# Optimization experiments

Hardware: AMD Instinct MI355X
Metric: run time of the kernel (lower is better)

Reference implementation:

```python
import jax, jax.numpy as jnp
import numpy as np

HID = 512
HEADS = 8
HEAD_DIM = HID // HEADS
BS, SEQ = 4, 2048


def setup_inputs() -> dict:
    key = jax.random.key(0)
    ks = jax.random.split(key, 12)
    s = 0.02
    return {
        "query": jax.random.normal(ks[0], (BS, SEQ, HID), jnp.float32),
        "key": jax.random.normal(ks[1], (BS, SEQ, HID), jnp.float32),
        "value": jax.random.normal(ks[2], (BS, SEQ, HID), jnp.float32),
        "query_mask": jnp.ones((BS, SEQ), dtype=bool),
        "key_mask": jnp.ones((BS, SEQ), dtype=bool),
        "Wq": jax.random.normal(ks[3], (HID, HID), jnp.float32) * s,
        "bq": jnp.zeros((HID,), jnp.float32),
        "Wk": jax.random.normal(ks[4], (HID, HID), jnp.float32) * s,
        "bk": jnp.zeros((HID,), jnp.float32),
        "Wv": jax.random.normal(ks[5], (HID, HID), jnp.float32) * s,
        "bv": jnp.zeros((HID,), jnp.float32),
        "Wo": jax.random.normal(ks[6], (HID, HID), jnp.float32) * s,
        "bo": jnp.zeros((HID,), jnp.float32),
    }


def _mha(query, key, value, query_mask, key_mask, Wq, bq, Wk, bk, Wv, bv, Wo, bo):
    bs, q_len, _ = query.shape
    k_len = key.shape[1]
    scale = jnp.sqrt(jnp.asarray(HEAD_DIM, query.dtype))

    def proj(x, W, b):  # nn.Linear: x @ W^T + b, then split heads -> [b,h,s,d]
        y = jnp.einsum('bse,fe->bsf', x, W) + b
        return y.reshape(bs, -1, HEADS, HEAD_DIM).transpose(0, 2, 1, 3)

    q = proj(query, Wq, bq)
    k = proj(key, Wk, bk)
    v = proj(value, Wv, bv)

    energy = jnp.einsum('bhqd,bhkd->bhqk', q, k) / scale  # [b,h,q,k]
    neg = -jnp.finfo(energy.dtype).max

    pad_mask = query_mask[:, None, :, None] & key_mask[:, None, None, :]
    energy = jnp.where(pad_mask, energy, neg)

    # causal: mask positions where q_idx < k_idx
    causal = jnp.arange(q_len)[:, None] < jnp.arange(k_len)[None, :]
    energy = jnp.where(causal[None, None], neg, energy)

    attn = jax.nn.softmax(energy, axis=-1)  # dropout p=0.0 -> identity
    x = jnp.einsum('bhqk,bhkd->bhqd', attn, v)
    x = x.transpose(0, 2, 1, 3).reshape(bs, q_len, HID)
    return jnp.einsum('bse,fe->bsf', x, Wo) + bo


def reference(query, key, value, query_mask, key_mask, Wq, bq, Wk, bk, Wv, bv, Wo, bo):
    return _mha(query, key, value, query_mask, key_mask, Wq, bq, Wk, bk, Wv, bv, Wo, bo)
```

## Files before the change

### kernel.cpp

```cpp
#include <hip/hip_runtime.h>
#include <hip/hip_bf16.h>

#define DEVI __device__ __forceinline__

typedef __attribute__((ext_vector_type(4)))  float f32x4;
typedef __attribute__((ext_vector_type(16))) float f32x16;
typedef __attribute__((ext_vector_type(8)))  short bf16x8;

constexpr int BS    = 4;
constexpr int SEQ   = 2048;
constexpr int HID   = 512;
constexpr int HEADS = 8;
constexpr int HD    = 64;
constexpr int M     = BS * SEQ;

constexpr float QSCALE = 0.125f * 1.4426950408889634f;

DEVI ushort f2bf(float f) {
    union { float f; unsigned u; } a; a.f = f;
    unsigned r = a.u + 0x7fffu + ((a.u >> 16) & 1u);
    return (ushort)(r >> 16);
}

DEVI f32x4 mfma16(bf16x8 a, bf16x8 b, f32x4 c) {
    return __builtin_amdgcn_mfma_f32_16x16x32_bf16(a, b, c, 0, 0, 0);
}
DEVI f32x16 mfma32(bf16x8 a, bf16x8 b, f32x16 c) {
    return __builtin_amdgcn_mfma_f32_32x32x16_bf16(a, b, c, 0, 0, 0);
}

DEVI void gl_lds16(const ushort* g, ushort* l) {
    __builtin_amdgcn_global_load_lds(
        (const __attribute__((address_space(1))) void*)g,
        (__attribute__((address_space(3))) void*)l,
        16, 0, 0);
}

DEVI unsigned cvtpk(float lo, float hi) {
    unsigned r;
    asm("v_cvt_pk_bf16_f32 %0, %1, %2" : "=v"(r) : "v"(lo), "v"(hi));
    return r;
}

__global__ void cast_w(const float* __restrict__ wq, const float* __restrict__ wk,
                       const float* __restrict__ wv, const float* __restrict__ wo,
                       ushort* __restrict__ oq, ushort* __restrict__ ok,
                       ushort* __restrict__ ov, ushort* __restrict__ oo)
{
    const int NW4 = HID * HID / 4;
    int i = blockIdx.x * blockDim.x + threadIdx.x;
    const int a = i >> 16, j = i & (NW4 - 1);
    const float* src = (a == 0) ? wq : (a == 1) ? wk : (a == 2) ? wv : wo;
    ushort* dst = (a == 0) ? oq : (a == 1) ? ok : (a == 2) ? ov : oo;
    float4 f = ((const float4*)src)[j];
    ushort4 u;
    u.x = f2bf(f.x); u.y = f2bf(f.y); u.z = f2bf(f.z); u.w = f2bf(f.w);
    ((ushort4*)dst)[j] = u;
}

template<bool AF32>
DEVI void gemm_core(const void* __restrict__ Ain, const ushort* __restrict__ W,
                    const float* __restrict__ bias, void* __restrict__ out,
                    float scale, int mode, ushort* lA, ushort* lB)
{
    constexpr int BK = 32, NK = HID / BK;
    const int tid  = threadIdx.x;
    const int lane = tid & 63, w = tid >> 6;
    const int wm = w >> 2, wn = w & 3;
    const int l15 = lane & 15, lg = lane >> 4;
    const int m0 = blockIdx.x * 128, n0 = blockIdx.y * 128;
    const int srow = tid >> 2, sc8 = (tid & 3) * 8;

    f32x4 acc[4][2];
    #pragma unroll
    for (int i = 0; i < 4; i++)
        #pragma unroll
        for (int n = 0; n < 2; n++) acc[i][n] = f32x4{0.f, 0.f, 0.f, 0.f};

    if constexpr (AF32) {
        const float* A = (const float*)Ain;
        const float4* ap = (const float4*)(A + (size_t)(m0 + srow) * HID + sc8);
        const float4 a0 = ap[0], a1 = ap[1];
        union { unsigned u[4]; bf16x8 v; } p;
        p.u[0] = cvtpk(a0.x, a0.y); p.u[1] = cvtpk(a0.z, a0.w);
        p.u[2] = cvtpk(a1.x, a1.y); p.u[3] = cvtpk(a1.z, a1.w);
        *(bf16x8*)(lA + srow * 32 + sc8) = p.v;
    } else {
        gl_lds16((const ushort*)Ain + (size_t)(m0 + srow) * HID + sc8, lA + w * 512);
    }
    gl_lds16(W + (size_t)(n0 + srow) * HID + sc8, lB + w * 512);
    __syncthreads();

    int cur = 0;
    for (int k = 0; k < NK; ++k) {
        ushort* lAc = lA + cur * 4096;
        ushort* lBc = lB + cur * 4096;
        ushort* lAn = lA + (cur ^ 1) * 4096;
        ushort* lBn = lB + (cur ^ 1) * 4096;
        const int k1 = (k + 1) * BK;
        const bool more = (k + 1 < NK);

        float4 a0n, a1n;
        if (more) {
            if constexpr (AF32) {
                const float* A = (const float*)Ain;
                const float4* ap = (const float4*)(A + (size_t)(m0 + srow) * HID + k1 + sc8);
                a0n = ap[0]; a1n = ap[1];
            } else {
                gl_lds16((const ushort*)Ain + (size_t)(m0 + srow) * HID + k1 + sc8,
                         lAn + w * 512);
            }
            gl_lds16(W + (size_t)(n0 + srow) * HID + k1 + sc8, lBn + w * 512);
        }

        bf16x8 af[4], bfr[2];
        #pragma unroll
        for (int i = 0; i < 4; i++)
            af[i] = *(const bf16x8*)(lAc + (wm * 64 + i * 16 + l15) * 32 + lg * 8);
        #pragma unroll
        for (int n = 0; n < 2; n++)
            bfr[n] = *(const bf16x8*)(lBc + (wn * 32 + n * 16 + l15) * 32 + lg * 8);
        #pragma unroll
        for (int i = 0; i < 4; i++)
            #pragma unroll
            for (int n = 0; n < 2; n++)
                acc[i][n] = mfma16(af[i], bfr[n], acc[i][n]);

        if (more) {
            if constexpr (AF32) {
                union { unsigned u[4]; bf16x8 v; } p;
                p.u[0] = cvtpk(a0n.x, a0n.y); p.u[1] = cvtpk(a0n.z, a0n.w);
                p.u[2] = cvtpk(a1n.x, a1n.y); p.u[3] = cvtpk(a1n.z, a1n.w);
                *(bf16x8*)(lAn + srow * 32 + sc8) = p.v;
            }
        }
        __syncthreads();
        cur ^= 1;
    }

    #pragma unroll
    for (int i = 0; i < 4; i++) {
        #pragma unroll
        for (int n = 0; n < 2; n++) {
            const int col = n0 + wn * 32 + n * 16 + l15;
            const float bb = bias[col];
            const int rbase = m0 + wm * 64 + i * 16 + lg * 4;
            #pragma unroll
            for (int jj = 0; jj < 4; jj++) {
                float v = (acc[i][n][jj] + bb) * scale;
                const int r = rbase + jj;
                if (mode == 3) {
                    ((float*)out)[(size_t)r * HID + col] = v;
                } else {
                    const int b = r >> 11, s = r & (SEQ - 1);
                    const int h = col >> 6, d = col & 63;
                    const int bh = b * HEADS + h;
                    const int t = s >> 5;
                    const ushort u = f2bf(v);
                    if (mode == 0) {
                        const int l31r = s & 31;
                        const int ds = d >> 4, hif = (d >> 3) & 1, jf = d & 7;
                        ((ushort*)out)[(((size_t)bh * 64 + t) * 4 + ds) * 512 +
                                       (hif * 32 + l31r) * 8 + jf] = u;
                    } else {
                        const int c = s & 31;
                        const int kvh = (c >> 4) & 1, hif = (c >> 2) & 1;
                        const int jf = (c & 3) + ((c >> 3) & 1) * 4;
                        const int dt = d >> 5, drow = d & 31;
                        ((ushort*)out)[(((size_t)bh * 64 + t) * 4 + dt * 2 + kvh) * 512 +
                                       (hif * 32 + drow) * 8 + jf] = u;
                    }
                }
            }
        }
    }
}

__global__ __launch_bounds__(512, 4)
void gemm_qkv(const float* __restrict__ Xq, const float* __restrict__ Xk,
              const float* __restrict__ Xv,
              const ushort* __restrict__ Wq, const ushort* __restrict__ Wk,
              const ushort* __restrict__ Wv,
              const float* __restrict__ bq, const float* __restrict__ bk,
              const float* __restrict__ bv,
              ushort* __restrict__ Qf, ushort* __restrict__ Kf,
              ushort* __restrict__ Vf)
{
    __shared__ ushort lA[2 * 128 * 32];
    __shared__ ushort lB[2 * 128 * 32];
    const int z = blockIdx.z;
    const float* A = z == 0 ? Xq : z == 1 ? Xk : Xv;
    const ushort* W = z == 0 ? Wq : z == 1 ? Wk : Wv;
    const float* bias = z == 0 ? bq : z == 1 ? bk : bv;
    void* out = z == 0 ? (void*)Qf : z == 1 ? (void*)Kf : (void*)Vf;
    gemm_core<true>(A, W, bias, out, z == 0 ? QSCALE : 1.0f, z == 2 ? 2 : 0, lA, lB);
}

__global__ __launch_bounds__(512, 4)
void gemm_o(const ushort* __restrict__ ctx, const ushort* __restrict__ Wo,
            const float* __restrict__ bo, float* __restrict__ out)
{
    __shared__ ushort lA[2 * 128 * 32];
    __shared__ ushort lB[2 * 128 * 32];
    gemm_core<false>(ctx, Wo, bo, out, 1.0f, 3, lA, lB);
}

__global__ __launch_bounds__(256)
void attn5(const ushort* __restrict__ Qf, const ushort* __restrict__ Kf,
           const ushort* __restrict__ Vf, ushort* __restrict__ ctx)
{
    __shared__ float part[4][2][16][64];
    __shared__ float pml[4][2][32];

    const int tid  = threadIdx.x;
    const int lane = tid & 63, w = tid >> 6;
    const int l31 = lane & 31, hi = lane >> 5;

    const int bid = blockIdx.x;
    const int bh  = bid & 31;
    const int qt  = 63 - (bid >> 5);
    const int qb  = qt * 32;

    const ushort* Qb = Qf + ((size_t)bh * 64 + qt) * 2048;
    const ushort* Kb = Kf + (size_t)bh * 64 * 2048;
    const ushort* Vb = Vf + (size_t)bh * 64 * 2048;

    bf16x8 qf[4];
    #pragma unroll
    for (int ds = 0; ds < 4; ds++)
        qf[ds] = *(const bf16x8*)(Qb + ds * 512 + lane * 8);

    f32x16 acc0 = {}, acc1 = {};
    float mrun = -3e38f, lrun = 0.f;

    bf16x8 kf[4] = {}, va[4] = {};
    if (w <= qt) {
        const ushort* kp = Kb + (size_t)w * 2048 + lane * 8;
        const ushort* vp = Vb + (size_t)w * 2048 + lane * 8;
        #pragma unroll
        for (int ds = 0; ds < 4; ds++) {
            kf[ds] = *(const bf16x8*)(kp + ds * 512);
            va[ds] = *(const bf16x8*)(vp + ds * 512);
        }
    }

    for (int t = w; t <= qt; t += 4) {
        f32x16 s = {};
        #pragma unroll
        for (int ds = 0; ds < 4; ds++)
            s = mfma32(kf[ds], qf[ds], s);

        bf16x8 kfn[4], van[4];
        {
            const int tn = (t + 4 <= qt) ? t + 4 : t;
            const ushort* kp = Kb + (size_t)tn * 2048 + lane * 8;
            const ushort* vp = Vb + (size_t)tn * 2048 + lane * 8;
            #pragma unroll
            for (int ds = 0; ds < 4; ds++) {
                kfn[ds] = *(const bf16x8*)(kp + ds * 512);
                van[ds] = *(const bf16x8*)(vp + ds * 512);
            }
        }

        if (t == qt) {
            #pragma unroll
            for (int r = 0; r < 16; r++) {
                const int kvrow = (r & 3) + 8 * (r >> 2) + 4 * hi;
                s[r] = (kvrow > l31) ? -3e38f : s[r];
            }
        }

        float m8[8];
        #pragma unroll
        for (int r = 0; r < 8; r++) m8[r] = fmaxf(s[r], s[r + 8]);
        float m4a = fmaxf(m8[0], m8[1]), m4b = fmaxf(m8[2], m8[3]);
        float m4c = fmaxf(m8[4], m8[5]), m4d = fmaxf(m8[6], m8[7]);
        float pmax = fmaxf(fmaxf(m4a, m4b), fmaxf(m4c, m4d));
        pmax = fmaxf(pmax, __shfl_xor(pmax, 32));

        if (!__all(pmax <= mrun + 8.f)) {
            const float mnew = fmaxf(mrun, pmax);
            const float corr = __builtin_amdgcn_exp2f(mrun - mnew);
            lrun *= corr;
            #pragma unroll
            for (int r = 0; r < 16; r++) { acc0[r] *= corr; acc1[r] *= corr; }
            mrun = mnew;
        }

        float e[16];
        #pragma unroll
        for (int r = 0; r < 16; r++)
            e[r] = __builtin_amdgcn_exp2f(s[r] - mrun);
        float es0 = (e[0] + e[1]) + (e[2] + e[3]);
        float es1 = (e[4] + e[5]) + (e[6] + e[7]);
        float es2 = (e[8] + e[9]) + (e[10] + e[11]);
        float es3 = (e[12] + e[13]) + (e[14] + e[15]);
        float esum = (es0 + es1) + (es2 + es3);
        lrun += esum + __shfl_xor(esum, 32);

        union { unsigned u[4]; bf16x8 v; } pb0, pb1;
        pb0.u[0] = cvtpk(e[0],  e[1]);  pb0.u[1] = cvtpk(e[2],  e[3]);
        pb0.u[2] = cvtpk(e[4],  e[5]);  pb0.u[3] = cvtpk(e[6],  e[7]);
        pb1.u[0] = cvtpk(e[8],  e[9]);  pb1.u[1] = cvtpk(e[10], e[11]);
        pb1.u[2] = cvtpk(e[12], e[13]); pb1.u[3] = cvtpk(e[14], e[15]);

        acc0 = mfma32(va[0], pb0.v, acc0);
        acc0 = mfma32(va[1], pb1.v, acc0);
        acc1 = mfma32(va[2], pb0.v, acc1);
        acc1 = mfma32(va[3], pb1.v, acc1);

        #pragma unroll
        for (int ds = 0; ds < 4; ds++) { kf[ds] = kfn[ds]; va[ds] = van[ds]; }
    }

    #pragma unroll
    for (int r = 0; r < 16; r++) {
        part[w][0][r][lane] = acc0[r];
        part[w][1][r][lane] = acc1[r];
    }
    if (hi == 0) { pml[w][0][l31] = mrun; pml[w][1][l31] = lrun; }
    __syncthreads();

    const float mm0 = pml[0][0][l31], ll0 = pml[0][1][l31];
    const float mm1 = pml[1][0][l31], ll1 = pml[1][1][l31];
    const float mm2 = pml[2][0][l31], ll2 = pml[2][1][l31];
    const float mm3 = pml[3][0][l31], ll3 = pml[3][1][l31];
    const float mstar = fmaxf(fmaxf(mm0, mm1), fmaxf(mm2, mm3));
    const float f0 = __builtin_amdgcn_exp2f(mm0 - mstar);
    const float f1 = __builtin_amdgcn_exp2f(mm1 - mstar);
    const float f2 = __builtin_amdgcn_exp2f(mm2 - mstar);
    const float f3 = __builtin_amdgcn_exp2f(mm3 - mstar);
    const float lstar = ll0 * f0 + ll1 * f1 + ll2 * f2 + ll3 * f3;
    const float inv = 1.f / lstar;

    const int b = bh >> 3, h = bh & 7;
    ushort* op = ctx + ((size_t)(b * SEQ + qb + l31)) * HID + h * HD;
    #pragma unroll
    for (int a = 0; a < 2; a++) {
        float v[4];
        #pragma unroll
        for (int j = 0; j < 4; j++) {
            const int r = 4 * w + j;
            v[j] = (part[0][a][r][lane] * f0 + part[1][a][r][lane] * f1 +
                    part[2][a][r][lane] * f2 + part[3][a][r][lane] * f3) * inv;
        }
        ushort4 o;
        o.x = f2bf(v[0]); o.y = f2bf(v[1]); o.z = f2bf(v[2]); o.w = f2bf(v[3]);
        *(ushort4*)(op + a * 32 + 8 * w + 4 * hi) = o;
    }
}

extern "C" void kernel_launch(void* const* d_in, const int* in_sizes, int n_in,
                              void* d_out, int out_size, void* d_ws, size_t ws_size,
                              hipStream_t stream) {
    const float* q  = (const float*)d_in[0];
    const float* k  = (const float*)d_in[1];
    const float* v  = (const float*)d_in[2];
    const float* Wq = (const float*)d_in[5];
    const float* bq = (const float*)d_in[6];
    const float* Wk = (const float*)d_in[7];
    const float* bk = (const float*)d_in[8];
    const float* Wv = (const float*)d_in[9];
    const float* bv = (const float*)d_in[10];
    const float* Wo = (const float*)d_in[11];
    const float* bo = (const float*)d_in[12];

    char* ws = (char*)d_ws;
    constexpr size_t XSZ = (size_t)M * HID * 2;
    constexpr size_t WSZ = (size_t)HID * HID * 2;
    ushort* Wqb = (ushort*)(ws);
    ushort* Wkb = (ushort*)(ws + WSZ);
    ushort* Wvb = (ushort*)(ws + 2 * WSZ);
    ushort* Wob = (ushort*)(ws + 3 * WSZ);
    ushort* Qf  = (ushort*)(ws + 4 * WSZ);
    ushort* Kf  = (ushort*)(ws + 4 * WSZ + XSZ);
    ushort* Vf  = (ushort*)(ws + 4 * WSZ + 2 * XSZ);
    ushort* ctx = (ushort*)(ws + 4 * WSZ + 3 * XSZ);

    cast_w<<<1024, 256, 0, stream>>>(Wq, Wk, Wv, Wo, Wqb, Wkb, Wvb, Wob);

    dim3 gqkv(M / 128, HID / 128, 3);
    gemm_qkv<<<gqkv, 512, 0, stream>>>(q, k, v, Wqb, Wkb, Wvb,
                                       bq, bk, bv, Qf, Kf, Vf);

    attn5<<<BS * HEADS * (SEQ / 32), 256, 0, stream>>>(Qf, Kf, Vf, ctx);

    dim3 go(M / 128, HID / 128);
    gemm_o<<<go, 512, 0, stream>>>(ctx, Wob, bo, (float*)d_out);
}
```

Before: 91.62 us.

## Process two query tiles per attention block and restructure GEMM LDS pipeline

The attention kernel now handles a 64-row query strip (two 32-row tiles) per block, so each K/V tile loaded from global memory serves two query tiles. This halves the block count and cuts redundant K/V reads, at the cost of more registers and serialized epilogue passes. The GEMM core switches to a fragment-major LDS layout that matches the MFMA operand order, prefetches fp32 A two steps ahead, and replaces __syncthreads with explicit waitcnt plus s_barrier so global loads can stay in flight across iterations.

```diff
diff --git a/kernel.cpp b/kernel.cpp
--- a/kernel.cpp
+++ b/kernel.cpp
@@ -69,7 +69,14 @@
     const int wm = w >> 2, wn = w & 3;
     const int l15 = lane & 15, lg = lane >> 4;
     const int m0 = blockIdx.x * 128, n0 = blockIdx.y * 128;
-    const int srow = tid >> 2, sc8 = (tid & 3) * 8;
+    const int fr = lane & 15;
+    const int fc = (lane >> 4) * 8;
+
+    const ushort* Wrow = W + (size_t)(n0 + 16 * w + fr) * HID + fc;
+    const float*  Af   = (const float*)Ain;
+    const ushort* Ab   = (const ushort*)Ain;
+    const float*  Arow = Af + (size_t)(m0 + 16 * w + fr) * HID + fc;
+    const ushort* Abrow = Ab + (size_t)(m0 + 16 * w + fr) * HID + fc;
 
     f32x4 acc[4][2];
     #pragma unroll
@@ -77,19 +84,23 @@
         #pragma unroll
         for (int n = 0; n < 2; n++) acc[i][n] = f32x4{0.f, 0.f, 0.f, 0.f};
 
+    gl_lds16(Wrow, lB + w * 512);
+    float4 aR0, aR1;
     if constexpr (AF32) {
-        const float* A = (const float*)Ain;
-        const float4* ap = (const float4*)(A + (size_t)(m0 + srow) * HID + sc8);
-        const float4 a0 = ap[0], a1 = ap[1];
+        const float4* ap = (const float4*)Arow;
+        float4 a0 = ap[0], a1 = ap[1];
         union { unsigned u[4]; bf16x8 v; } p;
         p.u[0] = cvtpk(a0.x, a0.y); p.u[1] = cvtpk(a0.z, a0.w);
         p.u[2] = cvtpk(a1.x, a1.y); p.u[3] = cvtpk(a1.z, a1.w);
-        *(bf16x8*)(lA + srow * 32 + sc8) = p.v;
+        *(bf16x8*)(lA + tid * 8) = p.v;
+        const float4* ap1 = (const float4*)(Arow + BK);
+        aR0 = ap1[0]; aR1 = ap1[1];
+        asm volatile("s_waitcnt lgkmcnt(0)" ::: "memory");
     } else {
-        gl_lds16((const ushort*)Ain + (size_t)(m0 + srow) * HID + sc8, lA + w * 512);
-    }
-    gl_lds16(W + (size_t)(n0 + srow) * HID + sc8, lB + w * 512);
-    __syncthreads();
+        gl_lds16(Abrow, lA + w * 512);
+        asm volatile("s_waitcnt vmcnt(0) lgkmcnt(0)" ::: "memory");
+    }
+    __builtin_amdgcn_s_barrier();
 
     int cur = 0;
     for (int k = 0; k < NK; ++k) {
@@ -97,44 +108,44 @@
         ushort* lBc = lB + cur * 4096;
         ushort* lAn = lA + (cur ^ 1) * 4096;
         ushort* lBn = lB + (cur ^ 1) * 4096;
-        const int k1 = (k + 1) * BK;
-        const bool more = (k + 1 < NK);
-
-        float4 a0n, a1n;
-        if (more) {
-            if constexpr (AF32) {
-                const float* A = (const float*)Ain;
-                const float4* ap = (const float4*)(A + (size_t)(m0 + srow) * HID + k1 + sc8);
-                a0n = ap[0]; a1n = ap[1];
-            } else {
-                gl_lds16((const ushort*)Ain + (size_t)(m0 + srow) * HID + k1 + sc8,
-                         lAn + w * 512);
-            }
-            gl_lds16(W + (size_t)(n0 + srow) * HID + k1 + sc8, lBn + w * 512);
+        const bool moreB = (k + 1 < NK);
+        const bool moreA = AF32 && (k + 2 < NK);
+
+        if (moreB) gl_lds16(Wrow + (k + 1) * BK, lBn + w * 512);
+
+        if constexpr (AF32) {
+            if (moreB) {
+                union { unsigned u[4]; bf16x8 v; } p;
+                p.u[0] = cvtpk(aR0.x, aR0.y); p.u[1] = cvtpk(aR0.z, aR0.w);
+                p.u[2] = cvtpk(aR1.x, aR1.y); p.u[3] = cvtpk(aR1.z, aR1.w);
+                *(bf16x8*)(lAn + tid * 8) = p.v;
+            }
+            if (moreA) {
+                const float4* ap = (const float4*)(Arow + (k + 2) * BK);
+                aR0 = ap[0]; aR1 = ap[1];
+            }
+        } else {
+            if (moreB) gl_lds16(Abrow + (k + 1) * BK, lAn + w * 512);
         }
 
         bf16x8 af[4], bfr[2];
         #pragma unroll
         for (int i = 0; i < 4; i++)
-            af[i] = *(const bf16x8*)(lAc + (wm * 64 + i * 16 + l15) * 32 + lg * 8);
+            af[i] = *(const bf16x8*)(lAc + (wm * 4 + i) * 512 + lane * 8);
         #pragma unroll
         for (int n = 0; n < 2; n++)
-            bfr[n] = *(const bf16x8*)(lBc + (wn * 32 + n * 16 + l15) * 32 + lg * 8);
+            bfr[n] = *(const bf16x8*)(lBc + (wn * 2 + n) * 512 + lane * 8);
         #pragma unroll
         for (int i = 0; i < 4; i++)
             #pragma unroll
             for (int n = 0; n < 2; n++)
                 acc[i][n] = mfma16(af[i], bfr[n], acc[i][n]);
 
-        if (more) {
-            if constexpr (AF32) {
-                union { unsigned u[4]; bf16x8 v; } p;
-                p.u[0] = cvtpk(a0n.x, a0n.y); p.u[1] = cvtpk(a0n.z, a0n.w);
-                p.u[2] = cvtpk(a1n.x, a1n.y); p.u[3] = cvtpk(a1n.z, a1n.w);
-                *(bf16x8*)(lAn + srow * 32 + sc8) = p.v;
-            }
-        }
-        __syncthreads();
+        if (moreB) {
+            if (moreA) asm volatile("s_waitcnt vmcnt(2) lgkmcnt(0)" ::: "memory");
+            else       asm volatile("s_waitcnt vmcnt(0) lgkmcnt(0)" ::: "memory");
+            __builtin_amdgcn_s_barrier();
+        }
         cur ^= 1;
     }
 
@@ -186,8 +197,8 @@
               ushort* __restrict__ Qf, ushort* __restrict__ Kf,
               ushort* __restrict__ Vf)
 {
-    __shared__ ushort lA[2 * 128 * 32];
-    __shared__ ushort lB[2 * 128 * 32];
+    __shared__ ushort lA[2 * 8 * 512];
+    __shared__ ushort lB[2 * 8 * 512];
     const int z = blockIdx.z;
     const float* A = z == 0 ? Xq : z == 1 ? Xk : Xv;
     const ushort* W = z == 0 ? Wq : z == 1 ? Wk : Wv;
@@ -200,13 +211,13 @@
 void gemm_o(const ushort* __restrict__ ctx, const ushort* __restrict__ Wo,
             const float* __restrict__ bo, float* __restrict__ out)
 {
-    __shared__ ushort lA[2 * 128 * 32];
-    __shared__ ushort lB[2 * 128 * 32];
+    __shared__ ushort lA[2 * 8 * 512];
+    __shared__ ushort lB[2 * 8 * 512];
     gemm_core<false>(ctx, Wo, bo, out, 1.0f, 3, lA, lB);
 }
 
 __global__ __launch_bounds__(256)
-void attn5(const ushort* __restrict__ Qf, const ushort* __restrict__ Kf,
+void attn6(const ushort* __restrict__ Qf, const ushort* __restrict__ Kf,
            const ushort* __restrict__ Vf, ushort* __restrict__ ctx)
 {
     __shared__ float part[4][2][16][64];
@@ -218,135 +229,181 @@
 
     const int bid = blockIdx.x;
     const int bh  = bid & 31;
-    const int qt  = 63 - (bid >> 5);
-    const int qb  = qt * 32;
-
-    const ushort* Qb = Qf + ((size_t)bh * 64 + qt) * 2048;
+    const int strip = 31 - (bid >> 5);
+    const int qtA = strip * 2, qtB = qtA + 1;
+    const int qbase = strip * 64;
+
     const ushort* Kb = Kf + (size_t)bh * 64 * 2048;
     const ushort* Vb = Vf + (size_t)bh * 64 * 2048;
-
-    bf16x8 qf[4];
+    const ushort* QbA = Qf + ((size_t)bh * 64 + qtA) * 2048;
+    const ushort* QbB = QbA + 2048;
+
+    bf16x8 qfA[4], qfB[4];
     #pragma unroll
-    for (int ds = 0; ds < 4; ds++)
-        qf[ds] = *(const bf16x8*)(Qb + ds * 512 + lane * 8);
-
-    f32x16 acc0 = {}, acc1 = {};
-    float mrun = -3e38f, lrun = 0.f;
-
-    bf16x8 kf[4] = {}, va[4] = {};
-    if (w <= qt) {
+    for (int ds = 0; ds < 4; ds++) {
+        qfA[ds] = *(const bf16x8*)(QbA + ds * 512 + lane * 8);
+        qfB[ds] = *(const bf16x8*)(QbB + ds * 512 + lane * 8);
+    }
+
+    f32x16 a0A = {}, a1A = {}, a0B = {}, a1B = {};
+    float mA = -3e38f, lA_ = 0.f, mB = -3e38f, lB_ = 0.f;
+
+    bf16x8 kf[4] = {};
+    if (w <= qtB) {
         const ushort* kp = Kb + (size_t)w * 2048 + lane * 8;
-        const ushort* vp = Vb + (size_t)w * 2048 + lane * 8;
-        #pragma unroll
-        for (int ds = 0; ds < 4; ds++) {
-            kf[ds] = *(const bf16x8*)(kp + ds * 512);
-            va[ds] = *(const bf16x8*)(vp + ds * 512);
-        }
-    }
-
-    for (int t = w; t <= qt; t += 4) {
-        f32x16 s = {};
-        #pragma unroll
-        for (int ds = 0; ds < 4; ds++)
-            s = mfma32(kf[ds], qf[ds], s);
-
-        bf16x8 kfn[4], van[4];
+        #pragma unroll
+        for (int ds = 0; ds < 4; ds++) kf[ds] = *(const bf16x8*)(kp + ds * 512);
+    }
+
+    for (int t = w; t <= qtB; t += 4) {
+        const bool doA = (t <= qtA);
+
+        f32x16 sB = {};
+        #pragma unroll
+        for (int ds = 0; ds < 4; ds++) sB = mfma32(kf[ds], qfB[ds], sB);
+
+        bf16x8 va[4], kfn[4];
         {
-            const int tn = (t + 4 <= qt) ? t + 4 : t;
+            const ushort* vp = Vb + (size_t)t * 2048 + lane * 8;
+            const int tn = (t + 4 <= qtB) ? t + 4 : t;
             const ushort* kp = Kb + (size_t)tn * 2048 + lane * 8;
-            const ushort* vp = Vb + (size_t)tn * 2048 + lane * 8;
             #pragma unroll
             for (int ds = 0; ds < 4; ds++) {
+                va[ds]  = *(const bf16x8*)(vp + ds * 512);
                 kfn[ds] = *(const bf16x8*)(kp + ds * 512);
-                van[ds] = *(const bf16x8*)(vp + ds * 512);
-            }
-        }
-
-        if (t == qt) {
+            }
+        }
+
+        if (t == qtB) {
             #pragma unroll
             for (int r = 0; r < 16; r++) {
                 const int kvrow = (r & 3) + 8 * (r >> 2) + 4 * hi;
-                s[r] = (kvrow > l31) ? -3e38f : s[r];
-            }
-        }
-
-        float m8[8];
-        #pragma unroll
-        for (int r = 0; r < 8; r++) m8[r] = fmaxf(s[r], s[r + 8]);
-        float m4a = fmaxf(m8[0], m8[1]), m4b = fmaxf(m8[2], m8[3]);
-        float m4c = fmaxf(m8[4], m8[5]), m4d = fmaxf(m8[6], m8[7]);
-        float pmax = fmaxf(fmaxf(m4a, m4b), fmaxf(m4c, m4d));
-        pmax = fmaxf(pmax, __shfl_xor(pmax, 32));
-
-        if (!__all(pmax <= mrun + 8.f)) {
-            const float mnew = fmaxf(mrun, pmax);
-            const float corr = __builtin_amdgcn_exp2f(mrun - mnew);
-            lrun *= corr;
-            #pragma unroll
-            for (int r = 0; r < 16; r++) { acc0[r] *= corr; acc1[r] *= corr; }
-            mrun = mnew;
-        }
-
-        float e[16];
-        #pragma unroll
-        for (int r = 0; r < 16; r++)
-            e[r] = __builtin_amdgcn_exp2f(s[r] - mrun);
-        float es0 = (e[0] + e[1]) + (e[2] + e[3]);
-        float es1 = (e[4] + e[5]) + (e[6] + e[7]);
-        float es2 = (e[8] + e[9]) + (e[10] + e[11]);
-        float es3 = (e[12] + e[13]) + (e[14] + e[15]);
-        float esum = (es0 + es1) + (es2 + es3);
-        lrun += esum + __shfl_xor(esum, 32);
-
-        union { unsigned u[4]; bf16x8 v; } pb0, pb1;
-        pb0.u[0] = cvtpk(e[0],  e[1]);  pb0.u[1] = cvtpk(e[2],  e[3]);
-        pb0.u[2] = cvtpk(e[4],  e[5]);  pb0.u[3] = cvtpk(e[6],  e[7]);
-        pb1.u[0] = cvtpk(e[8],  e[9]);  pb1.u[1] = cvtpk(e[10], e[11]);
-        pb1.u[2] = cvtpk(e[12], e[13]); pb1.u[3] = cvtpk(e[14], e[15]);
-
-        acc0 = mfma32(va[0], pb0.v, acc0);
-        acc0 = mfma32(va[1], pb1.v, acc0);
-        acc1 = mfma32(va[2], pb0.v, acc1);
-        acc1 = mfma32(va[3], pb1.v, acc1);
-
-        #pragma unroll
-        for (int ds = 0; ds < 4; ds++) { kf[ds] = kfn[ds]; va[ds] = van[ds]; }
-    }
-
+                sB[r] = (kvrow > l31) ? -3e38f : sB[r];
+            }
+        }
+
+        union { unsigned u[4]; bf16x8 v; } pb0B, pb1B;
+        {
+            float m8[8];
+            #pragma unroll
+            for (int r = 0; r < 8; r++) m8[r] = fmaxf(sB[r], sB[r + 8]);
+            float pmax = fmaxf(fmaxf(fmaxf(m8[0], m8[1]), fmaxf(m8[2], m8[3])),
+                               fmaxf(fmaxf(m8[4], m8[5]), fmaxf(m8[6], m8[7])));
+            pmax = fmaxf(pmax, __shfl_xor(pmax, 32));
+            if (!__all(pmax <= mB + 8.f)) {
+                const float mnew = fmaxf(mB, pmax);
+                const float corr = __builtin_amdgcn_exp2f(mB - mnew);
+                lB_ *= corr;
+                #pragma unroll
+                for (int r = 0; r < 16; r++) { a0B[r] *= corr; a1B[r] *= corr; }
+                mB = mnew;
+            }
+            float e[16];
+            #pragma unroll
+            for (int r = 0; r < 16; r++) e[r] = __builtin_amdgcn_exp2f(sB[r] - mB);
+            float es = ((e[0]+e[1])+(e[2]+e[3])) + ((e[4]+e[5])+(e[6]+e[7]))
+                     + ((e[8]+e[9])+(e[10]+e[11])) + ((e[12]+e[13])+(e[14]+e[15]));
+            lB_ += es + __shfl_xor(es, 32);
+            pb0B.u[0] = cvtpk(e[0],  e[1]);  pb0B.u[1] = cvtpk(e[2],  e[3]);
+            pb0B.u[2] = cvtpk(e[4],  e[5]);  pb0B.u[3] = cvtpk(e[6],  e[7]);
+            pb1B.u[0] = cvtpk(e[8],  e[9]);  pb1B.u[1] = cvtpk(e[10], e[11]);
+            pb1B.u[2] = cvtpk(e[12], e[13]); pb1B.u[3] = cvtpk(e[14], e[15]);
+        }
+
+        union { unsigned u[4]; bf16x8 v; } pb0A, pb1A;
+        if (doA) {
+            f32x16 sA = {};
+            #pragma unroll
+            for (int ds = 0; ds < 4; ds++) sA = mfma32(kf[ds], qfA[ds], sA);
+            if (t == qtA) {
+                #pragma unroll
+                for (int r = 0; r < 16; r++) {
+                    const int kvrow = (r & 3) + 8 * (r >> 2) + 4 * hi;
+                    sA[r] = (kvrow > l31) ? -3e38f : sA[r];
+                }
+            }
+            float m8[8];
+            #pragma unroll
+            for (int r = 0; r < 8; r++) m8[r] = fmaxf(sA[r], sA[r + 8]);
+            float pmax = fmaxf(fmaxf(fmaxf(m8[0], m8[1]), fmaxf(m8[2], m8[3])),
+                               fmaxf(fmaxf(m8[4], m8[5]), fmaxf(m8[6], m8[7])));
+            pmax = fmaxf(pmax, __shfl_xor(pmax, 32));
+            if (!__all(pmax <= mA + 8.f)) {
+                const float mnew = fmaxf(mA, pmax);
+                const float corr = __builtin_amdgcn_exp2f(mA - mnew);
+                lA_ *= corr;
+                #pragma unroll
+                for (int r = 0; r < 16; r++) { a0A[r] *= corr; a1A[r] *= corr; }
+                mA = mnew;
+            }
+            float e[16];
+            #pragma unroll
+            for (int r = 0; r < 16; r++) e[r] = __builtin_amdgcn_exp2f(sA[r] - mA);
+            float es = ((e[0]+e[1])+(e[2]+e[3])) + ((e[4]+e[5])+(e[6]+e[7]))
+                     + ((e[8]+e[9])+(e[10]+e[11])) + ((e[12]+e[13])+(e[14]+e[15]));
+            lA_ += es + __shfl_xor(es, 32);
+            pb0A.u[0] = cvtpk(e[0],  e[1]);  pb0A.u[1] = cvtpk(e[2],  e[3]);
+            pb0A.u[2] = cvtpk(e[4],  e[5]);  pb0A.u[3] = cvtpk(e[6],  e[7]);
+            pb1A.u[0] = cvtpk(e[8],  e[9]);  pb1A.u[1] = cvtpk(e[10], e[11]);
+            pb1A.u[2] = cvtpk(e[12], e[13]); pb1A.u[3] = cvtpk(e[14], e[15]);
+        }
+
+        a0B = mfma32(va[0], pb0B.v, a0B);
+        a0B = mfma32(va[1], pb1B.v, a0B);
+        a1B = mfma32(va[2], pb0B.v, a1B);
+        a1B = mfma32(va[3], pb1B.v, a1B);
+        if (doA) {
+            a0A = mfma32(va[0], pb0A.v, a0A);
+            a0A = mfma32(va[1], pb1A.v, a0A);
+            a1A = mfma32(va[2], pb0A.v, a1A);
+            a1A = mfma32(va[3], pb1A.v, a1A);
+        }
+
+        #pragma unroll
+        for (int ds = 0; ds < 4; ds++) kf[ds] = kfn[ds];
+    }
+
+    const int b = bh >> 3, h = bh & 7;
     #pragma unroll
-    for (int r = 0; r < 16; r++) {
-        part[w][0][r][lane] = acc0[r];
-        part[w][1][r][lane] = acc1[r];
-    }
-    if (hi == 0) { pml[w][0][l31] = mrun; pml[w][1][l31] = lrun; }
-    __syncthreads();
-
-    const float mm0 = pml[0][0][l31], ll0 = pml[0][1][l31];
-    const float mm1 = pml[1][0][l31], ll1 = pml[1][1][l31];
-    const float mm2 = pml[2][0][l31], ll2 = pml[2][1][l31];
-    const float mm3 = pml[3][0][l31], ll3 = pml[3][1][l31];
-    const float mstar = fmaxf(fmaxf(mm0, mm1), fmaxf(mm2, mm3));
-    const float f0 = __builtin_amdgcn_exp2f(mm0 - mstar);
-    const float f1 = __builtin_amdgcn_exp2f(mm1 - mstar);
-    const float f2 = __builtin_amdgcn_exp2f(mm2 - mstar);
-    const float f3 = __builtin_amdgcn_exp2f(mm3 - mstar);
-    const float lstar = ll0 * f0 + ll1 * f1 + ll2 * f2 + ll3 * f3;
-    const float inv = 1.f / lstar;
-
-    const int b = bh >> 3, h = bh & 7;
-    ushort* op = ctx + ((size_t)(b * SEQ + qb + l31)) * HID + h * HD;
-    #pragma unroll
-    for (int a = 0; a < 2; a++) {
-        float v[4];
-        #pragma unroll
-        for (int j = 0; j < 4; j++) {
-            const int r = 4 * w + j;
-            v[j] = (part[0][a][r][lane] * f0 + part[1][a][r][lane] * f1 +
-                    part[2][a][r][lane] * f2 + part[3][a][r][lane] * f3) * inv;
-        }
-        ushort4 o;
-        o.x = f2bf(v[0]); o.y = f2bf(v[1]); o.z = f2bf(v[2]); o.w = f2bf(v[3]);
-        *(ushort4*)(op + a * 32 + 8 * w + 4 * hi) = o;
+    for (int pass = 0; pass < 2; pass++) {
+        const f32x16& p0 = pass ? a0B : a0A;
+        const f32x16& p1 = pass ? a1B : a1A;
+        const float mr = pass ? mB : mA;
+        const float lr = pass ? lB_ : lA_;
+        #pragma unroll
+        for (int r = 0; r < 16; r++) {
+            part[w][0][r][lane] = p0[r];
+            part[w][1][r][lane] = p1[r];
+        }
+        if (hi == 0) { pml[w][0][l31] = mr; pml[w][1][l31] = lr; }
+        __syncthreads();
+
+        const float mm0 = pml[0][0][l31], ll0 = pml[0][1][l31];
+        const float mm1 = pml[1][0][l31], ll1 = pml[1][1][l31];
+        const float mm2 = pml[2][0][l31], ll2 = pml[2][1][l31];
+        const float mm3 = pml[3][0][l31], ll3 = pml[3][1][l31];
+        const float mstar = fmaxf(fmaxf(mm0, mm1), fmaxf(mm2, mm3));
+        const float f0 = __builtin_amdgcn_exp2f(mm0 - mstar);
+        const float f1 = __builtin_amdgcn_exp2f(mm1 - mstar);
+        const float f2 = __builtin_amdgcn_exp2f(mm2 - mstar);
+        const float f3 = __builtin_amdgcn_exp2f(mm3 - mstar);
+        const float inv = 1.f / (ll0 * f0 + ll1 * f1 + ll2 * f2 + ll3 * f3);
+
+        ushort* op = ctx + ((size_t)(b * SEQ + qbase + pass * 32 + l31)) * HID + h * HD;
+        #pragma unroll
+        for (int a = 0; a < 2; a++) {
+            float v[4];
+            #pragma unroll
+            for (int j = 0; j < 4; j++) {
+                const int r = 4 * w + j;
+                v[j] = (part[0][a][r][lane] * f0 + part[1][a][r][lane] * f1 +
+                        part[2][a][r][lane] * f2 + part[3][a][r][lane] * f3) * inv;
+            }
+            ushort4 o;
+            o.x = f2bf(v[0]); o.y = f2bf(v[1]); o.z = f2bf(v[2]); o.w = f2bf(v[3]);
+            *(ushort4*)(op + a * 32 + 8 * w + 4 * hi) = o;
+        }
+        __syncthreads();
     }
 }
 
@@ -383,7 +440,7 @@
     gemm_qkv<<<gqkv, 512, 0, stream>>>(q, k, v, Wqb, Wkb, Wvb,
                                        bq, bk, bv, Qf, Kf, Vf);
 
-    attn5<<<BS * HEADS * (SEQ / 32), 256, 0, stream>>>(Qf, Kf, Vf, ctx);
+    attn6<<<BS * HEADS * (SEQ / 64), 256, 0, stream>>>(Qf, Kf, Vf, ctx);
 
     dim3 go(M / 128, HID / 128);
     gemm_o<<<go, 512, 0, stream>>>(ctx, Wob, bo, (float*)d_out);
```

Result: slower. 115.3 us (+25.9%).
